# Optimization experiments

Measured on AMD Instinct MI355X. Metric: run time of the kernel, lower is better.

## Reference

```python
import jax, jax.numpy as jnp
import numpy as np

N_HEADS = 4
HEAD_DIM = 64
N_EXPERTS = 64
TOP_K = 2
INPUT_DIM = 2048
N_TOKENS = 16384


def setup_inputs() -> dict:
    key = jax.random.key(0)
    ks = jax.random.split(key, 10)
    s = 0.02
    return {
        "x": jax.random.normal(ks[0], (N_TOKENS, INPUT_DIM), dtype=jnp.float32),
        "Wp": jax.random.normal(ks[1], (INPUT_DIM, N_HEADS * HEAD_DIM), dtype=jnp.float32) * s,
        "bp": jnp.zeros((N_HEADS * HEAD_DIM,), dtype=jnp.float32),
        "W1": jax.random.normal(ks[2], (N_HEADS, HEAD_DIM, HEAD_DIM), dtype=jnp.float32) * s,
        "b1": jnp.zeros((N_HEADS, HEAD_DIM), dtype=jnp.float32),
        "W2": jax.random.normal(ks[3], (N_HEADS, HEAD_DIM, N_EXPERTS), dtype=jnp.float32) * s,
        "b2": jnp.zeros((N_HEADS, N_EXPERTS), dtype=jnp.float32),
        "Wc": jax.random.normal(ks[4], (N_HEADS * N_EXPERTS, N_EXPERTS), dtype=jnp.float32) * s,
        "bc": jnp.zeros((N_EXPERTS,), dtype=jnp.float32),
        "temperature": jnp.ones((1,), dtype=jnp.float32) * 2.0,
        "noise_scale": jnp.ones((1,), dtype=jnp.float32) * 0.1,
    }


def reference(x, Wp, bp, W1, b1, W2, b2, Wc, bc, temperature, noise_scale):
    # eval-mode forward (no dropout, no routing noise)
    n = x.shape[0]
    h = (x @ Wp + bp).reshape(n, N_HEADS, HEAD_DIM)            # [N, 4, 64]
    hid = jax.nn.relu(jnp.einsum('nhd,hde->nhe', h, W1) + b1)   # [N, 4, 64]
    head_logits = jnp.einsum('nhd,hde->nhe', hid, W2) + b2      # [N, 4, E] (cat order = head order)
    combined = head_logits.reshape(n, N_HEADS * N_EXPERTS)      # [N, 4*E]
    gate_logits = combined @ Wc + bc                            # [N, E]
    gate_logits = gate_logits / jnp.clip(temperature, 0.5, 5.0)
    top_vals, top_idx = jax.lax.top_k(gate_logits, TOP_K)       # [N, k]
    top_gates = jax.nn.softmax(top_vals, axis=-1)
    gates = jnp.zeros_like(gate_logits).at[jnp.arange(n)[:, None], top_idx].set(top_gates)
    return gates, top_idx, gate_logits
```

## Files before the change

kernel.cpp:

```cpp
#include <hip/hip_runtime.h>
#include <math.h>

#define NT   16384
#define KD   2048
#define PROJ 256
#define NH   4
#define HD   64
#define NE   64

#define GATES_OFF 0
#define IDX_OFF   (NT * NE)
#define GL_OFF    (NT * NE + NT * 2)

typedef __attribute__((ext_vector_type(8))) short short8;
typedef __attribute__((ext_vector_type(4))) float f32x4;

static __device__ __forceinline__ ushort f2bf_rne(float f) {
    uint u = __float_as_uint(f);
    u += 0x7FFFu + ((u >> 16) & 1u);
    return (ushort)(u >> 16);
}
static __device__ __forceinline__ float bf2f(ushort b) {
    return __uint_as_float(((uint)b) << 16);
}

__global__ __launch_bounds__(256) void k0_split(const float* __restrict__ Wp,
                                                ushort* __restrict__ WpT_hi,
                                                ushort* __restrict__ WpT_lo)
{
    const int tid = blockIdx.x * 256 + threadIdx.x;
#pragma unroll
    for (int e = 0; e < 4; ++e) {
        const int idx = tid + e * 131072;
        const int k = idx >> 8, c = idx & 255;
        const float v = Wp[idx];
        const ushort hi = f2bf_rne(v);
        const ushort lo = f2bf_rne(v - bf2f(hi));
        WpT_hi[(size_t)c * KD + k] = hi;
        WpT_lo[(size_t)c * KD + k] = lo;
    }
}

__global__ __launch_bounds__(256) void k1_mfma(const float* __restrict__ x,
                                               const ushort* __restrict__ WpT_hi,
                                               const ushort* __restrict__ WpT_lo,
                                               const float* __restrict__ bp,
                                               float* __restrict__ hT)
{
    __shared__ ushort Ah[2][4096], Al[2][4096];

    const int t   = threadIdx.x;
    const int wid = t >> 6;
    const int wm4 = (wid >> 1) * 4;
    const int wn  = wid & 1;
    const int l   = t & 63;
    const int m0  = blockIdx.x * 128;
    const int n0  = blockIdx.y * 128;

    const int s0 = t, s1 = t + 256;
    const float* xa0 = &x[(size_t)(m0 + 16 * (s0 >> 6) + (s0 & 15)) * KD + ((s0 >> 4) & 3) * 8];
    const float* xa1 = &x[(size_t)(m0 + 16 * (s1 >> 6) + (s1 & 15)) * KD + ((s1 >> 4) & 3) * 8];

    const ushort* wph = &WpT_hi[(size_t)(n0 + wn * 64 + (l & 15)) * KD + (l >> 4) * 8];
    const ushort* wpl = &WpT_lo[(size_t)(n0 + wn * 64 + (l & 15)) * KD + (l >> 4) * 8];

    f32x4 acc[4][4];
#pragma unroll
    for (int m = 0; m < 4; ++m)
#pragma unroll
        for (int n = 0; n < 4; ++n) acc[m][n] = (f32x4){0.f, 0.f, 0.f, 0.f};

#define K1_STAGE_SLOT(DH, DL, VA, VB)                                          \
    {                                                                          \
        const float ff[8] = { (VA).x, (VA).y, (VA).z, (VA).w,                  \
                              (VB).x, (VB).y, (VB).z, (VB).w };                \
        uint hp[4], lp[4];                                                     \
        _Pragma("unroll")                                                      \
        for (int i = 0; i < 4; ++i) {                                          \
            const uint u0 = __float_as_uint(ff[2 * i]);                        \
            const uint u1 = __float_as_uint(ff[2 * i + 1]);                    \
            hp[i] = (u0 >> 16) | (u1 & 0xFFFF0000u);                           \
            const float r0 = ff[2 * i]     - __uint_as_float(u0 & 0xFFFF0000u);\
            const float r1 = ff[2 * i + 1] - __uint_as_float(u1 & 0xFFFF0000u);\
            lp[i] = (__float_as_uint(r0) >> 16) |                              \
                    (__float_as_uint(r1) & 0xFFFF0000u);                       \
        }                                                                      \
        *(uint4*)(DH) = (uint4){hp[0], hp[1], hp[2], hp[3]};                   \
        *(uint4*)(DL) = (uint4){lp[0], lp[1], lp[2], lp[3]};                   \
    }

#define K1_STAGE(BUF, R0, R1, R2, R3)                                          \
    K1_STAGE_SLOT(&Ah[BUF][s0 * 8], &Al[BUF][s0 * 8], R0, R1);                 \
    K1_STAGE_SLOT(&Ah[BUF][s1 * 8], &Al[BUF][s1 * 8], R2, R3);

#define K1_LOADA(KB, R0, R1, R2, R3)                                           \
    R0 = *(const float4*)(xa0 + (KB));                                         \
    R1 = *(const float4*)(xa0 + (KB) + 4);                                     \
    R2 = *(const float4*)(xa1 + (KB));                                         \
    R3 = *(const float4*)(xa1 + (KB) + 4);

#define K1_LOADB(KB, BH, BL)                                                   \
    _Pragma("unroll")                                                          \
    for (int n = 0; n < 4; ++n) {                                              \
        BH[n] = *(const short8*)(wph + (size_t)n * 16 * KD + (KB));            \
        BL[n] = *(const short8*)(wpl + (size_t)n * 16 * KD + (KB));            \
    }

#define K1_MFMA(BUF, BH, BL)                                                   \
    _Pragma("unroll")                                                          \
    for (int m = 0; m < 4; ++m) {                                              \
        const short8 ah = *(const short8*)&Ah[BUF][((wm4 + m) * 64 + l) * 8];  \
        const short8 al = *(const short8*)&Al[BUF][((wm4 + m) * 64 + l) * 8];  \
        _Pragma("unroll")                                                      \
        for (int n = 0; n < 4; ++n) {                                          \
            acc[m][n] = __builtin_amdgcn_mfma_f32_16x16x32_bf16(ah, BH[n], acc[m][n], 0, 0, 0); \
            acc[m][n] = __builtin_amdgcn_mfma_f32_16x16x32_bf16(ah, BL[n], acc[m][n], 0, 0, 0); \
            acc[m][n] = __builtin_amdgcn_mfma_f32_16x16x32_bf16(al, BH[n], acc[m][n], 0, 0, 0); \
        }                                                                      \
    }

    float4 xA0, xA1, xA2, xA3, xB0, xB1, xB2, xB3;
    short8 bhA[4], blA[4], bhB[4], blB[4];

    K1_LOADA(0, xA0, xA1, xA2, xA3);
    K1_LOADB(0, bhA, blA);

    for (int tp = 0; tp < 32; ++tp) {
        const int kb1 = (2 * tp + 1) * 32;
        const int kb2 = (2 * tp + 2) * 32;
        K1_STAGE(0, xA0, xA1, xA2, xA3);
        __syncthreads();
        K1_LOADA(kb1, xB0, xB1, xB2, xB3);
        K1_LOADB(kb1, bhB, blB);
        K1_MFMA(0, bhA, blA);
        K1_STAGE(1, xB0, xB1, xB2, xB3);
        __syncthreads();
        if (tp + 1 < 32) {
            K1_LOADA(kb2, xA0, xA1, xA2, xA3);
            K1_LOADB(kb2, bhA, blA);
        }
        K1_MFMA(1, bhB, blB);
    }

#pragma unroll
    for (int n = 0; n < 4; ++n) {
        const int col = n0 + wn * 64 + n * 16 + (l & 15);
        const float b = bp[col];
#pragma unroll
        for (int m = 0; m < 4; ++m) {
            const int tok = m0 + wm4 * 16 + m * 16 + (l >> 4) * 4;
            float4 st = { acc[m][n].x + b, acc[m][n].y + b,
                          acc[m][n].z + b, acc[m][n].w + b };
            *(float4*)&hT[(size_t)col * NT + tok] = st;
        }
    }
#undef K1_STAGE_SLOT
#undef K1_STAGE
#undef K1_LOADA
#undef K1_LOADB
#undef K1_MFMA
}

__global__ __launch_bounds__(256) void k2_heads(const float* __restrict__ hT,
                                                const float* __restrict__ W1,
                                                const float* __restrict__ b1,
                                                const float* __restrict__ W2,
                                                const float* __restrict__ b2,
                                                float* __restrict__ hlT)
{
    __shared__ float W1s[64][64];
    __shared__ float W2s[64][64];
    __shared__ float Hs[64][132];

    const int t    = threadIdx.x;
    const int eg   = t & 15;
    const int tg   = t >> 4;
    const int head = blockIdx.y;
    const int tok0 = blockIdx.x * 128;

    {
        const float4* g1 = (const float4*)(W1 + (size_t)head * HD * HD);
        const float4* g2 = (const float4*)(W2 + (size_t)head * HD * HD);
        float4* s1 = (float4*)&W1s[0][0];
        float4* s2 = (float4*)&W2s[0][0];
#pragma unroll
        for (int q = 0; q < 4; ++q) {
            s1[t + q * 256] = g1[t + q * 256];
            s2[t + q * 256] = g2[t + q * 256];
        }
    }
    const float4 b1v = *(const float4*)&b1[head * HD + eg * 4];
    const float4 b2v = *(const float4*)&b2[head * HD + eg * 4];
    __syncthreads();

    float acc[4][8];
    {
        const float bb[4] = { b1v.x, b1v.y, b1v.z, b1v.w };
#pragma unroll
        for (int j = 0; j < 4; ++j)
#pragma unroll
            for (int i = 0; i < 8; ++i) acc[j][i] = bb[j];
    }
    const float* hbase = &hT[(size_t)(head * HD) * NT + tok0 + tg * 8];
#pragma unroll 4
    for (int d = 0; d < HD; ++d) {
        const float4 w  = *(const float4*)&W1s[d][eg * 4];
        const float4 h0 = *(const float4*)&hbase[(size_t)d * NT];
        const float4 h1 = *(const float4*)&hbase[(size_t)d * NT + 4];
        const float wv[4] = { w.x, w.y, w.z, w.w };
        const float hv[8] = { h0.x, h0.y, h0.z, h0.w, h1.x, h1.y, h1.z, h1.w };
#pragma unroll
        for (int j = 0; j < 4; ++j)
#pragma unroll
            for (int i = 0; i < 8; ++i)
                acc[j][i] = fmaf(wv[j], hv[i], acc[j][i]);
    }
#pragma unroll
    for (int j = 0; j < 4; ++j) {
        float4 lo, hi;
        lo.x = fmaxf(acc[j][0], 0.f); lo.y = fmaxf(acc[j][1], 0.f);
        lo.z = fmaxf(acc[j][2], 0.f); lo.w = fmaxf(acc[j][3], 0.f);
        hi.x = fmaxf(acc[j][4], 0.f); hi.y = fmaxf(acc[j][5], 0.f);
        hi.z = fmaxf(acc[j][6], 0.f); hi.w = fmaxf(acc[j][7], 0.f);
        *(float4*)&Hs[eg * 4 + j][tg * 8]     = lo;
        *(float4*)&Hs[eg * 4 + j][tg * 8 + 4] = hi;
    }
    __syncthreads();

    {
        const float bb[4] = { b2v.x, b2v.y, b2v.z, b2v.w };
#pragma unroll
        for (int j = 0; j < 4; ++j)
#pragma unroll
            for (int i = 0; i < 8; ++i) acc[j][i] = bb[j];
    }
#pragma unroll 4
    for (int d = 0; d < HD; ++d) {
        const float4 w  = *(const float4*)&W2s[d][eg * 4];
        const float4 h0 = *(const float4*)&Hs[d][tg * 8];
        const float4 h1 = *(const float4*)&Hs[d][tg * 8 + 4];
        const float wv[4] = { w.x, w.y, w.z, w.w };
        const float hv[8] = { h0.x, h0.y, h0.z, h0.w, h1.x, h1.y, h1.z, h1.w };
#pragma unroll
        for (int j = 0; j < 4; ++j)
#pragma unroll
            for (int i = 0; i < 8; ++i)
                acc[j][i] = fmaf(wv[j], hv[i], acc[j][i]);
    }
#pragma unroll
    for (int j = 0; j < 4; ++j) {
        float4 lo = { acc[j][0], acc[j][1], acc[j][2], acc[j][3] };
        float4 hi = { acc[j][4], acc[j][5], acc[j][6], acc[j][7] };
        float* dst = &hlT[(size_t)(head * HD + eg * 4 + j) * NT + tok0 + tg * 8];
        *(float4*)&dst[0] = lo;
        *(float4*)&dst[4] = hi;
    }
}

__global__ __launch_bounds__(512) void k3_gate(const float* __restrict__ hlT,
                                               const float* __restrict__ Wc,
                                               const float* __restrict__ bc,
                                               const float* __restrict__ temp,
                                               float* __restrict__ out)
{
    const int t    = threadIdx.x;
    const int eg   = t & 15;
    const int tg   = t >> 4;
    const int tok0 = blockIdx.x * 64;

    const float tv  = fminf(fmaxf(temp[0], 0.5f), 5.0f);
    const float inv = 1.0f / tv;
    const float4 bcv = *(const float4*)&bc[eg * 4];

    float acc[4][2];
    acc[0][0] = bcv.x; acc[0][1] = bcv.x;
    acc[1][0] = bcv.y; acc[1][1] = bcv.y;
    acc[2][0] = bcv.z; acc[2][1] = bcv.z;
    acc[3][0] = bcv.w; acc[3][1] = bcv.w;

    const float* hb = &hlT[tok0 + tg * 2];
#pragma unroll 8
    for (int k = 0; k < PROJ; ++k) {
        const float2 hv = *(const float2*)&hb[(size_t)k * NT];
        const float4 wv = *(const float4*)&Wc[k * NE + eg * 4];
        const float wa[4] = { wv.x, wv.y, wv.z, wv.w };
#pragma unroll
        for (int j = 0; j < 4; ++j) {
            acc[j][0] = fmaf(wa[j], hv.x, acc[j][0]);
            acc[j][1] = fmaf(wa[j], hv.y, acc[j][1]);
        }
    }

#pragma unroll
    for (int i = 0; i < 2; ++i) {
        const int tok = tok0 + tg * 2 + i;
        float gl_[4];
#pragma unroll
        for (int j = 0; j < 4; ++j) gl_[j] = acc[j][i] * inv;

        float v1 = gl_[0]; int i1 = eg * 4;
#pragma unroll
        for (int j = 1; j < 4; ++j)
            if (gl_[j] > v1) { v1 = gl_[j]; i1 = eg * 4 + j; }
#pragma unroll
        for (int off = 8; off >= 1; off >>= 1) {
            const float ov = __shfl_xor(v1, off);
            const int   oi = __shfl_xor(i1, off);
            if (ov > v1 || (ov == v1 && oi < i1)) { v1 = ov; i1 = oi; }
        }
        float v2 = -INFINITY; int i2 = NE;
#pragma unroll
        for (int j = 0; j < 4; ++j) {
            const int e = eg * 4 + j;
            if (e != i1 && gl_[j] > v2) { v2 = gl_[j]; i2 = e; }
        }
#pragma unroll
        for (int off = 8; off >= 1; off >>= 1) {
            const float ov = __shfl_xor(v2, off);
            const int   oi = __shfl_xor(i2, off);
            if (ov > v2 || (ov == v2 && oi < i2)) { v2 = ov; i2 = oi; }
        }

        const float e2  = expf(v2 - v1);
        const float s   = 1.f + e2;
        const float g1v = 1.f / s;
        const float g2v = e2 / s;

        float4 gv;
        {
            const int e0 = eg * 4;
            gv.x = (e0 + 0 == i1) ? g1v : ((e0 + 0 == i2) ? g2v : 0.f);
            gv.y = (e0 + 1 == i1) ? g1v : ((e0 + 1 == i2) ? g2v : 0.f);
            gv.z = (e0 + 2 == i1) ? g1v : ((e0 + 2 == i2) ? g2v : 0.f);
            gv.w = (e0 + 3 == i1) ? g1v : ((e0 + 3 == i2) ? g2v : 0.f);
        }
        *(float4*)&out[GATES_OFF + (size_t)tok * NE + eg * 4] = gv;
        const float4 glv = { gl_[0], gl_[1], gl_[2], gl_[3] };
        *(float4*)&out[GL_OFF + (size_t)tok * NE + eg * 4] = glv;
        if (eg == 0) {
            out[IDX_OFF + (size_t)tok * 2 + 0] = (float)i1;
            out[IDX_OFF + (size_t)tok * 2 + 1] = (float)i2;
        }
    }
}

extern "C" void kernel_launch(void* const* d_in, const int* in_sizes, int n_in,
                              void* d_out, int out_size, void* d_ws, size_t ws_size,
                              hipStream_t stream)
{
    (void)in_sizes; (void)n_in; (void)out_size; (void)ws_size;

    const float* x    = (const float*)d_in[0];
    const float* Wp   = (const float*)d_in[1];
    const float* bp   = (const float*)d_in[2];
    const float* W1   = (const float*)d_in[3];
    const float* b1   = (const float*)d_in[4];
    const float* W2   = (const float*)d_in[5];
    const float* b2   = (const float*)d_in[6];
    const float* Wc   = (const float*)d_in[7];
    const float* bc   = (const float*)d_in[8];
    const float* temp = (const float*)d_in[9];

    float* out = (float*)d_out;
    float* hT  = (float*)d_ws;
    float* hlT = hT + (size_t)PROJ * NT;

    ushort* WpT_hi = (ushort*)hlT;
    ushort* WpT_lo = WpT_hi + (size_t)KD * PROJ;

    k0_split<<<dim3(512),            256, 0, stream>>>(Wp, WpT_hi, WpT_lo);
    k1_mfma <<<dim3(NT / 128, 2),    256, 0, stream>>>(x, WpT_hi, WpT_lo, bp, hT);
    k2_heads<<<dim3(NT / 128, NH),   256, 0, stream>>>(hT, W1, b1, W2, b2, hlT);
    k3_gate <<<dim3(NT / 64),        512, 0, stream>>>(hlT, Wc, bc, temp, out);
}
```

Measured before the change: 229.7 us.

## Tile Wp transpose through LDS and halve GEMM N-tile for more blocks

```diff
diff --git a/kernel.cpp b/kernel.cpp
--- a/kernel.cpp
+++ b/kernel.cpp
@@ -28,24 +28,45 @@
                                                 ushort* __restrict__ WpT_hi,
                                                 ushort* __restrict__ WpT_lo)
 {
-    const int tid = blockIdx.x * 256 + threadIdx.x;
-#pragma unroll
-    for (int e = 0; e < 4; ++e) {
-        const int idx = tid + e * 131072;
-        const int k = idx >> 8, c = idx & 255;
-        const float v = Wp[idx];
-        const ushort hi = f2bf_rne(v);
-        const ushort lo = f2bf_rne(v - bf2f(hi));
-        WpT_hi[(size_t)c * KD + k] = hi;
-        WpT_lo[(size_t)c * KD + k] = lo;
-    }
-}
-
-__global__ __launch_bounds__(256) void k1_mfma(const float* __restrict__ x,
-                                               const ushort* __restrict__ WpT_hi,
-                                               const ushort* __restrict__ WpT_lo,
-                                               const float* __restrict__ bp,
-                                               float* __restrict__ hT)
+    __shared__ ushort Th[64][72];
+    __shared__ ushort Tl[64][72];
+
+    const int t  = threadIdx.x;
+    const int kb = blockIdx.x * 64;
+    const int cb = blockIdx.y * 64;
+
+#pragma unroll
+    for (int q = 0; q < 4; ++q) {
+        const int s   = t + q * 256;
+        const int row = s >> 4;
+        const int c4  = (s & 15) * 4;
+        const float4 v = *(const float4*)&Wp[(size_t)(kb + row) * PROJ + cb + c4];
+        const float vv[4] = { v.x, v.y, v.z, v.w };
+#pragma unroll
+        for (int j = 0; j < 4; ++j) {
+            const ushort hi = f2bf_rne(vv[j]);
+            const ushort lo = f2bf_rne(vv[j] - bf2f(hi));
+            Th[c4 + j][row] = hi;
+            Tl[c4 + j][row] = lo;
+        }
+    }
+    __syncthreads();
+
+#pragma unroll
+    for (int q = 0; q < 2; ++q) {
+        const int s    = t + q * 256;
+        const int crow = s >> 3;
+        const int kq   = (s & 7) * 8;
+        *(uint4*)&WpT_hi[(size_t)(cb + crow) * KD + kb + kq] = *(const uint4*)&Th[crow][kq];
+        *(uint4*)&WpT_lo[(size_t)(cb + crow) * KD + kb + kq] = *(const uint4*)&Tl[crow][kq];
+    }
+}
+
+__global__ __launch_bounds__(256, 2) void k1_mfma(const float* __restrict__ x,
+                                                  const ushort* __restrict__ WpT_hi,
+                                                  const ushort* __restrict__ WpT_lo,
+                                                  const float* __restrict__ bp,
+                                                  float* __restrict__ hT)
 {
     __shared__ ushort Ah[2][4096], Al[2][4096];
 
@@ -55,20 +76,20 @@
     const int wn  = wid & 1;
     const int l   = t & 63;
     const int m0  = blockIdx.x * 128;
-    const int n0  = blockIdx.y * 128;
+    const int n0  = blockIdx.y * 64;
 
     const int s0 = t, s1 = t + 256;
     const float* xa0 = &x[(size_t)(m0 + 16 * (s0 >> 6) + (s0 & 15)) * KD + ((s0 >> 4) & 3) * 8];
     const float* xa1 = &x[(size_t)(m0 + 16 * (s1 >> 6) + (s1 & 15)) * KD + ((s1 >> 4) & 3) * 8];
 
-    const ushort* wph = &WpT_hi[(size_t)(n0 + wn * 64 + (l & 15)) * KD + (l >> 4) * 8];
-    const ushort* wpl = &WpT_lo[(size_t)(n0 + wn * 64 + (l & 15)) * KD + (l >> 4) * 8];
-
-    f32x4 acc[4][4];
+    const ushort* wph = &WpT_hi[(size_t)(n0 + wn * 32 + (l & 15)) * KD + (l >> 4) * 8];
+    const ushort* wpl = &WpT_lo[(size_t)(n0 + wn * 32 + (l & 15)) * KD + (l >> 4) * 8];
+
+    f32x4 acc[4][2];
 #pragma unroll
     for (int m = 0; m < 4; ++m)
 #pragma unroll
-        for (int n = 0; n < 4; ++n) acc[m][n] = (f32x4){0.f, 0.f, 0.f, 0.f};
+        for (int n = 0; n < 2; ++n) acc[m][n] = (f32x4){0.f, 0.f, 0.f, 0.f};
 
 #define K1_STAGE_SLOT(DH, DL, VA, VB)                                          \
     {                                                                          \
@@ -101,7 +122,7 @@
 
 #define K1_LOADB(KB, BH, BL)                                                   \
     _Pragma("unroll")                                                          \
-    for (int n = 0; n < 4; ++n) {                                              \
+    for (int n = 0; n < 2; ++n) {                                              \
         BH[n] = *(const short8*)(wph + (size_t)n * 16 * KD + (KB));            \
         BL[n] = *(const short8*)(wpl + (size_t)n * 16 * KD + (KB));            \
     }
@@ -112,7 +133,7 @@
         const short8 ah = *(const short8*)&Ah[BUF][((wm4 + m) * 64 + l) * 8];  \
         const short8 al = *(const short8*)&Al[BUF][((wm4 + m) * 64 + l) * 8];  \
         _Pragma("unroll")                                                      \
-        for (int n = 0; n < 4; ++n) {                                          \
+        for (int n = 0; n < 2; ++n) {                                          \
             acc[m][n] = __builtin_amdgcn_mfma_f32_16x16x32_bf16(ah, BH[n], acc[m][n], 0, 0, 0); \
             acc[m][n] = __builtin_amdgcn_mfma_f32_16x16x32_bf16(ah, BL[n], acc[m][n], 0, 0, 0); \
             acc[m][n] = __builtin_amdgcn_mfma_f32_16x16x32_bf16(al, BH[n], acc[m][n], 0, 0, 0); \
@@ -120,7 +141,7 @@
     }
 
     float4 xA0, xA1, xA2, xA3, xB0, xB1, xB2, xB3;
-    short8 bhA[4], blA[4], bhB[4], blB[4];
+    short8 bhA[2], blA[2], bhB[2], blB[2];
 
     K1_LOADA(0, xA0, xA1, xA2, xA3);
     K1_LOADB(0, bhA, blA);
@@ -143,8 +164,8 @@
     }
 
 #pragma unroll
-    for (int n = 0; n < 4; ++n) {
-        const int col = n0 + wn * 64 + n * 16 + (l & 15);
+    for (int n = 0; n < 2; ++n) {
+        const int col = n0 + wn * 32 + n * 16 + (l & 15);
         const float b = bp[col];
 #pragma unroll
         for (int m = 0; m < 4; ++m) {
@@ -368,8 +389,8 @@
     ushort* WpT_hi = (ushort*)hlT;
     ushort* WpT_lo = WpT_hi + (size_t)KD * PROJ;
 
-    k0_split<<<dim3(512),            256, 0, stream>>>(Wp, WpT_hi, WpT_lo);
-    k1_mfma <<<dim3(NT / 128, 2),    256, 0, stream>>>(x, WpT_hi, WpT_lo, bp, hT);
-    k2_heads<<<dim3(NT / 128, NH),   256, 0, stream>>>(hT, W1, b1, W2, b2, hlT);
-    k3_gate <<<dim3(NT / 64),        512, 0, stream>>>(hlT, Wc, bc, temp, out);
-}
+    k0_split<<<dim3(KD / 64, PROJ / 64), 256, 0, stream>>>(Wp, WpT_hi, WpT_lo);
+    k1_mfma <<<dim3(NT / 128, PROJ / 64), 256, 0, stream>>>(x, WpT_hi, WpT_lo, bp, hT);
+    k2_heads<<<dim3(NT / 128, NH),        256, 0, stream>>>(hT, W1, b1, W2, b2, hlT);
+    k3_gate <<<dim3(NT / 64),             512, 0, stream>>>(hlT, Wc, bc, temp, out);
+}
```

Result: faster. 219.5 us (-4.4%).
